# Performance work log

Hardware: AMD Instinct MI355X
Metric: run time of the kernel (lower is better)

Reference implementation:

```python
import jax, jax.numpy as jnp
import numpy as np

H, V, L = 1024, 50257, 512

def setup_inputs() -> dict:
    key = jax.random.key(0)
    ks = jax.random.split(key, 14)
    s = 0.02
    return {
        "input": jax.random.randint(ks[0], (1,), 0, V),
        "hidden": jax.random.normal(ks[1], (1, 1, H), jnp.float32),
        "encoder_outputs": jax.random.normal(ks[2], (L, H), jnp.float32),
        "emb": jax.random.normal(ks[3], (V, H), jnp.float32) * s,
        "attn_w": jax.random.normal(ks[4], (L, 2 * H), jnp.float32) * s,
        "attn_b": jnp.zeros((L,), jnp.float32),
        "comb_w": jax.random.normal(ks[5], (H, 2 * H), jnp.float32) * s,
        "comb_b": jnp.zeros((H,), jnp.float32),
        "w_ih": jax.random.normal(ks[6], (3 * H, H), jnp.float32) * s,
        "w_hh": jax.random.normal(ks[7], (3 * H, H), jnp.float32) * s,
        "b_ih": jnp.zeros((3 * H,), jnp.float32),
        "b_hh": jnp.zeros((3 * H,), jnp.float32),
        "out_w": jax.random.normal(ks[8], (V, H), jnp.float32) * s,
        "out_b": jnp.zeros((V,), jnp.float32),
    }

def reference(input, hidden, encoder_outputs, emb, attn_w, attn_b,
              comb_w, comb_b, w_ih, w_hh, b_ih, b_hh, out_w, out_b):
    # embedding lookup (dropout is identity in eval mode)
    e = emb[input]                       # (1, H)
    h0 = hidden[0]                       # (1, H)
    # attention over encoder outputs
    scores = jnp.concatenate([e, h0], axis=1) @ attn_w.T + attn_b   # (1, L)
    attn_weights = jax.nn.softmax(scores, axis=1)                    # (1, L)
    attn_applied = attn_weights @ encoder_outputs                    # (1, H)
    # combine + relu
    x = jnp.concatenate([e, attn_applied], axis=1) @ comb_w.T + comb_b
    x = jax.nn.relu(x)                   # (1, H)
    # single GRU step (PyTorch gate layout: r, z, n)
    gi = x @ w_ih.T + b_ih               # (1, 3H)
    gh = h0 @ w_hh.T + b_hh              # (1, 3H)
    i_r, i_z, i_n = jnp.split(gi, 3, axis=1)
    h_r, h_z, h_n = jnp.split(gh, 3, axis=1)
    r = jax.nn.sigmoid(i_r + h_r)
    z = jax.nn.sigmoid(i_z + h_z)
    n = jnp.tanh(i_n + r * h_n)
    h_new = (1.0 - z) * n + z * h0       # (1, H)
    # output projection + log_softmax
    logits = h_new @ out_w.T + out_b     # (1, V)
    out = jax.nn.log_softmax(logits, axis=1)
    return out, h_new[None], attn_weights
```

## Files before the change

### kernel.cpp

```cpp
#include <hip/hip_runtime.h>

#define H 1024
#define L 512
#define V 50257

__device__ __forceinline__ float wave_reduce_sum(float v) {
    #pragma unroll
    for (int o = 32; o > 0; o >>= 1) v += __shfl_xor(v, o, 64);
    return v;
}

__device__ __forceinline__ float block_reduce_sum256(float v, float* lds) {
    v = wave_reduce_sum(v);
    int wid = threadIdx.x >> 6, lane = threadIdx.x & 63;
    if (lane == 0) lds[wid] = v;
    __syncthreads();
    float r = 0.f;
    if (threadIdx.x == 0) r = lds[0] + lds[1] + lds[2] + lds[3];
    __syncthreads();
    return r;
}

__global__ void k_scores(const float* __restrict__ emb, const int* __restrict__ input,
                         const float* __restrict__ hidden, const float* __restrict__ attn_w,
                         const float* __restrict__ attn_b, float* __restrict__ scores) {
    __shared__ float lds[4];
    int l = blockIdx.x, t = threadIdx.x;
    size_t erow = (size_t)input[0] * H;
    const float4* w = (const float4*)(attn_w + (size_t)l * 2 * H);
    float4 a  = w[t];
    float4 b  = w[256 + t];
    float4 ev = ((const float4*)(emb + erow))[t];
    float4 hv = ((const float4*)hidden)[t];
    float acc = a.x*ev.x + a.y*ev.y + a.z*ev.z + a.w*ev.w
              + b.x*hv.x + b.y*hv.y + b.z*hv.z + b.w*hv.w;
    acc = block_reduce_sum256(acc, lds);
    if (t == 0) scores[l] = acc + attn_b[l];
}

__global__ void k_softmax(const float* __restrict__ scores, float* __restrict__ attn_out) {
    __shared__ float lds[8];
    int t = threadIdx.x;
    float x = scores[t];
    float m = x;
    #pragma unroll
    for (int o = 32; o > 0; o >>= 1) m = fmaxf(m, __shfl_xor(m, o, 64));
    if ((t & 63) == 0) lds[t >> 6] = m;
    __syncthreads();
    m = lds[0];
    #pragma unroll
    for (int i = 1; i < 8; ++i) m = fmaxf(m, lds[i]);
    __syncthreads();
    float e = expf(x - m);
    float s = e;
    #pragma unroll
    for (int o = 32; o > 0; o >>= 1) s += __shfl_xor(s, o, 64);
    if ((t & 63) == 0) lds[t >> 6] = s;
    __syncthreads();
    s = 0.f;
    #pragma unroll
    for (int i = 0; i < 8; ++i) s += lds[i];
    attn_out[t] = e / s;
}

__global__ void k_attn_partial(const float* __restrict__ enc, const float* __restrict__ w,
                               float* __restrict__ partial) {
    int b = blockIdx.x, t = threadIdx.x;
    float4 acc = {0.f, 0.f, 0.f, 0.f};
    for (int l = b * 16; l < b * 16 + 16; ++l) {
        float wl = w[l];
        float4 ev = ((const float4*)(enc + (size_t)l * H))[t];
        acc.x += wl * ev.x; acc.y += wl * ev.y; acc.z += wl * ev.z; acc.w += wl * ev.w;
    }
    ((float4*)(partial + (size_t)b * H))[t] = acc;
}

__global__ void k_attn_reduce(const float* __restrict__ partial, float* __restrict__ attn_applied) {
    int h = blockIdx.x * 256 + threadIdx.x;
    float s = 0.f;
    #pragma unroll 8
    for (int p = 0; p < 32; ++p) s += partial[p * H + h];
    attn_applied[h] = s;
}

__global__ void k_combine(const float* __restrict__ emb, const int* __restrict__ input,
                          const float* __restrict__ attn_applied, const float* __restrict__ comb_w,
                          const float* __restrict__ comb_b, float* __restrict__ x) {
    __shared__ float lds[4];
    int h = blockIdx.x, t = threadIdx.x;
    size_t erow = (size_t)input[0] * H;
    const float4* w = (const float4*)(comb_w + (size_t)h * 2 * H);
    float4 a  = w[t];
    float4 b  = w[256 + t];
    float4 ev = ((const float4*)(emb + erow))[t];
    float4 av = ((const float4*)attn_applied)[t];
    float acc = a.x*ev.x + a.y*ev.y + a.z*ev.z + a.w*ev.w
              + b.x*av.x + b.y*av.y + b.z*av.z + b.w*av.w;
    acc = block_reduce_sum256(acc, lds);
    if (t == 0) x[h] = fmaxf(acc + comb_b[h], 0.f);
}

__global__ void k_gigh(const float* __restrict__ w_ih, const float* __restrict__ w_hh,
                       const float* __restrict__ b_ih, const float* __restrict__ b_hh,
                       const float* __restrict__ x, const float* __restrict__ hidden,
                       float* __restrict__ gi, float* __restrict__ gh) {
    __shared__ float lds[4];
    int j = blockIdx.x, t = threadIdx.x;
    float4 wi = ((const float4*)(w_ih + (size_t)j * H))[t];
    float4 wh = ((const float4*)(w_hh + (size_t)j * H))[t];
    float4 xv = ((const float4*)x)[t];
    float4 hv = ((const float4*)hidden)[t];
    float ai = wi.x*xv.x + wi.y*xv.y + wi.z*xv.z + wi.w*xv.w;
    float ah = wh.x*hv.x + wh.y*hv.y + wh.z*hv.z + wh.w*hv.w;
    ai = block_reduce_sum256(ai, lds);
    ah = block_reduce_sum256(ah, lds);
    if (t == 0) { gi[j] = ai + b_ih[j]; gh[j] = ah + b_hh[j]; }
}

__global__ void k_gru(const float* __restrict__ gi, const float* __restrict__ gh,
                      const float* __restrict__ hidden, float* __restrict__ hnew) {
    int h = blockIdx.x * 256 + threadIdx.x;
    float r = 1.f / (1.f + expf(-(gi[h] + gh[h])));
    float z = 1.f / (1.f + expf(-(gi[H + h] + gh[H + h])));
    float n = tanhf(gi[2 * H + h] + r * gh[2 * H + h]);
    hnew[h] = (1.f - z) * n + z * hidden[h];
}

__global__ void k_logits(const float* __restrict__ out_w, const float* __restrict__ out_b,
                         const float* __restrict__ hvec, float* __restrict__ logits) {
    int lane = threadIdx.x & 63;
    int gwave = blockIdx.x * 4 + (threadIdx.x >> 6);
    int nwaves = gridDim.x * 4;
    float4 h4[4];
    #pragma unroll
    for (int j = 0; j < 4; ++j) h4[j] = ((const float4*)hvec)[j * 64 + lane];
    for (int r = gwave; r < V; r += nwaves) {
        const float4* row = (const float4*)(out_w + (size_t)r * H);
        float acc = 0.f;
        #pragma unroll
        for (int j = 0; j < 4; ++j) {
            float4 a = row[j * 64 + lane];
            acc += a.x*h4[j].x + a.y*h4[j].y + a.z*h4[j].z + a.w*h4[j].w;
        }
        acc = wave_reduce_sum(acc);
        if (lane == 0) logits[r] = acc + out_b[r];
    }
}

__global__ void k_lse_partial(const float* __restrict__ logits,
                              float* __restrict__ mpart, float* __restrict__ spart) {
    __shared__ float lm[4], ls[4];
    const int CH = (V + 63) / 64;
    int b = blockIdx.x, t = threadIdx.x;
    int start = b * CH, end = min(start + CH, V);
    float m = -INFINITY, s = 0.f;
    for (int v = start + t; v < end; v += 256) {
        float xv = logits[v];
        if (xv > m) { s = s * expf(m - xv) + 1.f; m = xv; }
        else s += expf(xv - m);
    }
    #pragma unroll
    for (int o = 32; o > 0; o >>= 1) {
        float m2 = __shfl_xor(m, o, 64), s2 = __shfl_xor(s, o, 64);
        float mm = fmaxf(m, m2);
        if (mm > -INFINITY) s = s * expf(m - mm) + s2 * expf(m2 - mm);
        m = mm;
    }
    int wid = t >> 6, lane = t & 63;
    if (lane == 0) { lm[wid] = m; ls[wid] = s; }
    __syncthreads();
    if (t == 0) {
        float M = fmaxf(fmaxf(lm[0], lm[1]), fmaxf(lm[2], lm[3]));
        float S = 0.f;
        if (M > -INFINITY) {
            #pragma unroll
            for (int i = 0; i < 4; ++i) S += ls[i] * expf(lm[i] - M);
        }
        mpart[b] = M; spart[b] = S;
    }
}

__global__ void k_finalize(const float* __restrict__ mpart, const float* __restrict__ spart,
                           float* __restrict__ out) {
    float m = -INFINITY;
    #pragma unroll 8
    for (int i = 0; i < 64; ++i) m = fmaxf(m, mpart[i]);
    float s = 0.f;
    #pragma unroll 8
    for (int i = 0; i < 64; ++i) s += spart[i] * expf(mpart[i] - m);
    float logZ = m + logf(s);
    int v = blockIdx.x * 256 + threadIdx.x;
    if (v < V) out[v] -= logZ;
}

extern "C" void kernel_launch(void* const* d_in, const int* in_sizes, int n_in,
                              void* d_out, int out_size, void* d_ws, size_t ws_size,
                              hipStream_t stream) {
    const int*   input  = (const int*)  d_in[0];
    const float* hidden = (const float*)d_in[1];
    const float* enc    = (const float*)d_in[2];
    const float* emb    = (const float*)d_in[3];
    const float* attn_w = (const float*)d_in[4];
    const float* attn_b = (const float*)d_in[5];
    const float* comb_w = (const float*)d_in[6];
    const float* comb_b = (const float*)d_in[7];
    const float* w_ih   = (const float*)d_in[8];
    const float* w_hh   = (const float*)d_in[9];
    const float* b_ih   = (const float*)d_in[10];
    const float* b_hh   = (const float*)d_in[11];
    const float* out_w  = (const float*)d_in[12];
    const float* out_b  = (const float*)d_in[13];

    float* out   = (float*)d_out;
    float* hnew  = out + V;
    float* attnw = out + V + H;

    float* ws           = (float*)d_ws;
    float* scores       = ws;
    float* partial      = ws + 512;
    float* attn_applied = ws + 33280;
    float* xbuf         = ws + 34304;
    float* gi           = ws + 35328;
    float* gh           = ws + 38400;
    float* mpart        = ws + 41472;
    float* spart        = ws + 41536;

    k_scores      <<<512, 256, 0, stream>>>(emb, input, hidden, attn_w, attn_b, scores);
    k_softmax     <<<1, 512, 0, stream>>>(scores, attnw);
    k_attn_partial<<<32, 256, 0, stream>>>(enc, attnw, partial);
    k_attn_reduce <<<4, 256, 0, stream>>>(partial, attn_applied);
    k_combine     <<<1024, 256, 0, stream>>>(emb, input, attn_applied, comb_w, comb_b, xbuf);
    k_gigh        <<<3072, 256, 0, stream>>>(w_ih, w_hh, b_ih, b_hh, xbuf, hidden, gi, gh);
    k_gru         <<<4, 256, 0, stream>>>(gi, gh, hidden, hnew);
    k_logits      <<<2048, 256, 0, stream>>>(out_w, out_b, hnew, out);
    k_lse_partial <<<64, 256, 0, stream>>>(out, mpart, spart);
    k_finalize    <<<(V + 255) / 256, 256, 0, stream>>>(mpart, spart, out);
}
```

Baseline: 71.25 us.

## Fuse attention softmax/apply, GRU gates, and logits with LSE partials

Cuts the pipeline from ten launches to six. Softmax and the attention-weighted sum go into one kernel where every block recomputes the softmax. The GRU gate matvecs and the cell update go into one kernel per hidden unit, and the per-block max/sum-exp is computed inside the logits kernel, so the separate LSE pass over the logits is gone. This removes launch gaps and extra global round trips. In exchange, the finalize kernel now reduces 2048 partials in every block, and each attention block redundantly redoes the softmax.

```diff
diff --git a/kernel.cpp b/kernel.cpp
--- a/kernel.cpp
+++ b/kernel.cpp
@@ -3,22 +3,12 @@
 #define H 1024
 #define L 512
 #define V 50257
+#define LOGIT_BLOCKS 2048
 
 __device__ __forceinline__ float wave_reduce_sum(float v) {
     #pragma unroll
     for (int o = 32; o > 0; o >>= 1) v += __shfl_xor(v, o, 64);
     return v;
-}
-
-__device__ __forceinline__ float block_reduce_sum256(float v, float* lds) {
-    v = wave_reduce_sum(v);
-    int wid = threadIdx.x >> 6, lane = threadIdx.x & 63;
-    if (lane == 0) lds[wid] = v;
-    __syncthreads();
-    float r = 0.f;
-    if (threadIdx.x == 0) r = lds[0] + lds[1] + lds[2] + lds[3];
-    __syncthreads();
-    return r;
 }
 
 __global__ void k_scores(const float* __restrict__ emb, const int* __restrict__ input,
@@ -34,53 +24,54 @@
     float4 hv = ((const float4*)hidden)[t];
     float acc = a.x*ev.x + a.y*ev.y + a.z*ev.z + a.w*ev.w
               + b.x*hv.x + b.y*hv.y + b.z*hv.z + b.w*hv.w;
-    acc = block_reduce_sum256(acc, lds);
-    if (t == 0) scores[l] = acc + attn_b[l];
-}
-
-__global__ void k_softmax(const float* __restrict__ scores, float* __restrict__ attn_out) {
-    __shared__ float lds[8];
-    int t = threadIdx.x;
-    float x = scores[t];
-    float m = x;
+    acc = wave_reduce_sum(acc);
+    int wid = t >> 6, lane = t & 63;
+    if (lane == 0) lds[wid] = acc;
+    __syncthreads();
+    if (t == 0) scores[l] = lds[0] + lds[1] + lds[2] + lds[3] + attn_b[l];
+}
+
+__global__ void k_attn(const float* __restrict__ scores, const float* __restrict__ enc,
+                       float* __restrict__ attn_out, float* __restrict__ attn_applied) {
+    __shared__ float w[512];
+    __shared__ float red[4];
+    __shared__ float acc_lds[256];
+    __shared__ float sM, sS;
+    int t = threadIdx.x, lane = t & 63, wid = t >> 6;
+    float s0 = scores[t], s1 = scores[t + 256];
+    float m = fmaxf(s0, s1);
     #pragma unroll
     for (int o = 32; o > 0; o >>= 1) m = fmaxf(m, __shfl_xor(m, o, 64));
-    if ((t & 63) == 0) lds[t >> 6] = m;
-    __syncthreads();
-    m = lds[0];
-    #pragma unroll
-    for (int i = 1; i < 8; ++i) m = fmaxf(m, lds[i]);
-    __syncthreads();
-    float e = expf(x - m);
-    float s = e;
-    #pragma unroll
-    for (int o = 32; o > 0; o >>= 1) s += __shfl_xor(s, o, 64);
-    if ((t & 63) == 0) lds[t >> 6] = s;
-    __syncthreads();
-    s = 0.f;
-    #pragma unroll
-    for (int i = 0; i < 8; ++i) s += lds[i];
-    attn_out[t] = e / s;
-}
-
-__global__ void k_attn_partial(const float* __restrict__ enc, const float* __restrict__ w,
-                               float* __restrict__ partial) {
-    int b = blockIdx.x, t = threadIdx.x;
-    float4 acc = {0.f, 0.f, 0.f, 0.f};
-    for (int l = b * 16; l < b * 16 + 16; ++l) {
-        float wl = w[l];
-        float4 ev = ((const float4*)(enc + (size_t)l * H))[t];
-        acc.x += wl * ev.x; acc.y += wl * ev.y; acc.z += wl * ev.z; acc.w += wl * ev.w;
-    }
-    ((float4*)(partial + (size_t)b * H))[t] = acc;
-}
-
-__global__ void k_attn_reduce(const float* __restrict__ partial, float* __restrict__ attn_applied) {
-    int h = blockIdx.x * 256 + threadIdx.x;
-    float s = 0.f;
+    if (lane == 0) red[wid] = m;
+    __syncthreads();
+    if (t == 0) sM = fmaxf(fmaxf(red[0], red[1]), fmaxf(red[2], red[3]));
+    __syncthreads();
+    float M = sM;
+    float e0 = expf(s0 - M), e1 = expf(s1 - M);
+    float s = e0 + e1;
+    s = wave_reduce_sum(s);
+    if (lane == 0) red[wid] = s;
+    __syncthreads();
+    if (t == 0) sS = red[0] + red[1] + red[2] + red[3];
+    __syncthreads();
+    float inv = 1.f / sS;
+    w[t] = e0 * inv; w[t + 256] = e1 * inv;
+    __syncthreads();
+    if (blockIdx.x == 0) { attn_out[t] = w[t]; attn_out[t + 256] = w[t + 256]; }
+    int col = blockIdx.x * 16 + (t & 15);
+    int rc  = t >> 4;
+    float acc = 0.f;
     #pragma unroll 8
-    for (int p = 0; p < 32; ++p) s += partial[p * H + h];
-    attn_applied[h] = s;
+    for (int l = rc; l < 512; l += 16)
+        acc += w[l] * enc[(size_t)l * H + col];
+    acc_lds[t] = acc;
+    __syncthreads();
+    #pragma unroll
+    for (int st = 128; st >= 16; st >>= 1) {
+        if (t < st) acc_lds[t] += acc_lds[t + st];
+        __syncthreads();
+    }
+    if (t < 16) attn_applied[blockIdx.x * 16 + t] = acc_lds[t];
 }
 
 __global__ void k_combine(const float* __restrict__ emb, const int* __restrict__ input,
@@ -96,44 +87,62 @@
     float4 av = ((const float4*)attn_applied)[t];
     float acc = a.x*ev.x + a.y*ev.y + a.z*ev.z + a.w*ev.w
               + b.x*av.x + b.y*av.y + b.z*av.z + b.w*av.w;
-    acc = block_reduce_sum256(acc, lds);
-    if (t == 0) x[h] = fmaxf(acc + comb_b[h], 0.f);
-}
-
-__global__ void k_gigh(const float* __restrict__ w_ih, const float* __restrict__ w_hh,
-                       const float* __restrict__ b_ih, const float* __restrict__ b_hh,
-                       const float* __restrict__ x, const float* __restrict__ hidden,
-                       float* __restrict__ gi, float* __restrict__ gh) {
-    __shared__ float lds[4];
-    int j = blockIdx.x, t = threadIdx.x;
-    float4 wi = ((const float4*)(w_ih + (size_t)j * H))[t];
-    float4 wh = ((const float4*)(w_hh + (size_t)j * H))[t];
+    acc = wave_reduce_sum(acc);
+    int wid = t >> 6, lane = t & 63;
+    if (lane == 0) lds[wid] = acc;
+    __syncthreads();
+    if (t == 0) x[h] = fmaxf(lds[0] + lds[1] + lds[2] + lds[3] + comb_b[h], 0.f);
+}
+
+__global__ void k_gru_fused(const float* __restrict__ w_ih, const float* __restrict__ w_hh,
+                            const float* __restrict__ b_ih, const float* __restrict__ b_hh,
+                            const float* __restrict__ x, const float* __restrict__ hidden,
+                            float* __restrict__ hnew) {
+    __shared__ float lds[4][6];
+    int h = blockIdx.x, t = threadIdx.x, lane = t & 63, wid = t >> 6;
     float4 xv = ((const float4*)x)[t];
     float4 hv = ((const float4*)hidden)[t];
-    float ai = wi.x*xv.x + wi.y*xv.y + wi.z*xv.z + wi.w*xv.w;
-    float ah = wh.x*hv.x + wh.y*hv.y + wh.z*hv.z + wh.w*hv.w;
-    ai = block_reduce_sum256(ai, lds);
-    ah = block_reduce_sum256(ah, lds);
-    if (t == 0) { gi[j] = ai + b_ih[j]; gh[j] = ah + b_hh[j]; }
-}
-
-__global__ void k_gru(const float* __restrict__ gi, const float* __restrict__ gh,
-                      const float* __restrict__ hidden, float* __restrict__ hnew) {
-    int h = blockIdx.x * 256 + threadIdx.x;
-    float r = 1.f / (1.f + expf(-(gi[h] + gh[h])));
-    float z = 1.f / (1.f + expf(-(gi[H + h] + gh[H + h])));
-    float n = tanhf(gi[2 * H + h] + r * gh[2 * H + h]);
-    hnew[h] = (1.f - z) * n + z * hidden[h];
-}
-
-__global__ void k_logits(const float* __restrict__ out_w, const float* __restrict__ out_b,
-                         const float* __restrict__ hvec, float* __restrict__ logits) {
-    int lane = threadIdx.x & 63;
-    int gwave = blockIdx.x * 4 + (threadIdx.x >> 6);
-    int nwaves = gridDim.x * 4;
+    const float* rows[6] = {
+        w_ih + (size_t)h * H, w_ih + (size_t)(H + h) * H, w_ih + (size_t)(2 * H + h) * H,
+        w_hh + (size_t)h * H, w_hh + (size_t)(H + h) * H, w_hh + (size_t)(2 * H + h) * H };
+    float acc[6];
+    #pragma unroll
+    for (int k = 0; k < 6; ++k) {
+        float4 wv = ((const float4*)rows[k])[t];
+        float4 v  = (k < 3) ? xv : hv;
+        acc[k] = wv.x*v.x + wv.y*v.y + wv.z*v.z + wv.w*v.w;
+        acc[k] = wave_reduce_sum(acc[k]);
+    }
+    if (lane == 0) {
+        #pragma unroll
+        for (int k = 0; k < 6; ++k) lds[wid][k] = acc[k];
+    }
+    __syncthreads();
+    if (t == 0) {
+        float g[6];
+        #pragma unroll
+        for (int k = 0; k < 6; ++k) g[k] = lds[0][k] + lds[1][k] + lds[2][k] + lds[3][k];
+        float ir = g[0] + b_ih[h],         hr = g[3] + b_hh[h];
+        float iz = g[1] + b_ih[H + h],     hz = g[4] + b_hh[H + h];
+        float in_ = g[2] + b_ih[2 * H + h], hn = g[5] + b_hh[2 * H + h];
+        float r = 1.f / (1.f + expf(-(ir + hr)));
+        float z = 1.f / (1.f + expf(-(iz + hz)));
+        float n = tanhf(in_ + r * hn);
+        hnew[h] = (1.f - z) * n + z * hidden[h];
+    }
+}
+
+__global__ void k_logits_lse(const float* __restrict__ out_w, const float* __restrict__ out_b,
+                             const float* __restrict__ hvec, float* __restrict__ logits,
+                             float* __restrict__ mpart, float* __restrict__ spart) {
+    __shared__ float lm[4], ls[4];
+    int lane = threadIdx.x & 63, wid = threadIdx.x >> 6;
+    int gwave = blockIdx.x * 4 + wid;
+    const int nwaves = LOGIT_BLOCKS * 4;
     float4 h4[4];
     #pragma unroll
     for (int j = 0; j < 4; ++j) h4[j] = ((const float4*)hvec)[j * 64 + lane];
+    float m = -INFINITY, s = 0.f;
     for (int r = gwave; r < V; r += nwaves) {
         const float4* row = (const float4*)(out_w + (size_t)r * H);
         float acc = 0.f;
@@ -143,54 +152,55 @@
             acc += a.x*h4[j].x + a.y*h4[j].y + a.z*h4[j].z + a.w*h4[j].w;
         }
         acc = wave_reduce_sum(acc);
-        if (lane == 0) logits[r] = acc + out_b[r];
-    }
-}
-
-__global__ void k_lse_partial(const float* __restrict__ logits,
-                              float* __restrict__ mpart, float* __restrict__ spart) {
-    __shared__ float lm[4], ls[4];
-    const int CH = (V + 63) / 64;
-    int b = blockIdx.x, t = threadIdx.x;
-    int start = b * CH, end = min(start + CH, V);
-    float m = -INFINITY, s = 0.f;
-    for (int v = start + t; v < end; v += 256) {
-        float xv = logits[v];
-        if (xv > m) { s = s * expf(m - xv) + 1.f; m = xv; }
-        else s += expf(xv - m);
-    }
-    #pragma unroll
-    for (int o = 32; o > 0; o >>= 1) {
-        float m2 = __shfl_xor(m, o, 64), s2 = __shfl_xor(s, o, 64);
-        float mm = fmaxf(m, m2);
-        if (mm > -INFINITY) s = s * expf(m - mm) + s2 * expf(m2 - mm);
-        m = mm;
-    }
-    int wid = t >> 6, lane = t & 63;
+        float logit = acc + out_b[r];
+        if (lane == 0) logits[r] = logit;
+        if (logit > m) { s = s * expf(m - logit) + 1.f; m = logit; }
+        else           { s += expf(logit - m); }
+    }
     if (lane == 0) { lm[wid] = m; ls[wid] = s; }
     __syncthreads();
-    if (t == 0) {
+    if (threadIdx.x == 0) {
         float M = fmaxf(fmaxf(lm[0], lm[1]), fmaxf(lm[2], lm[3]));
         float S = 0.f;
         if (M > -INFINITY) {
             #pragma unroll
             for (int i = 0; i < 4; ++i) S += ls[i] * expf(lm[i] - M);
         }
-        mpart[b] = M; spart[b] = S;
+        mpart[blockIdx.x] = M; spart[blockIdx.x] = S;
     }
 }
 
 __global__ void k_finalize(const float* __restrict__ mpart, const float* __restrict__ spart,
                            float* __restrict__ out) {
-    float m = -INFINITY;
-    #pragma unroll 8
-    for (int i = 0; i < 64; ++i) m = fmaxf(m, mpart[i]);
-    float s = 0.f;
-    #pragma unroll 8
-    for (int i = 0; i < 64; ++i) s += spart[i] * expf(mpart[i] - m);
-    float logZ = m + logf(s);
-    int v = blockIdx.x * 256 + threadIdx.x;
-    if (v < V) out[v] -= logZ;
+    __shared__ float lm[4], ls[4];
+    __shared__ float sLogZ;
+    int t = threadIdx.x, lane = t & 63, wid = t >> 6;
+    float m = -INFINITY, s = 0.f;
+    for (int i = t; i < LOGIT_BLOCKS; i += 256) {
+        float m2 = mpart[i], s2 = spart[i];
+        float mm = fmaxf(m, m2);
+        if (mm > -INFINITY) s = s * expf(m - mm) + s2 * expf(m2 - mm);
+        m = mm;
+    }
+    #pragma unroll
+    for (int o = 32; o > 0; o >>= 1) {
+        float m2 = __shfl_xor(m, o, 64), s2 = __shfl_xor(s, o, 64);
+        float mm = fmaxf(m, m2);
+        if (mm > -INFINITY) s = s * expf(m - mm) + s2 * expf(m2 - mm);
+        m = mm;
+    }
+    if (lane == 0) { lm[wid] = m; ls[wid] = s; }
+    __syncthreads();
+    if (t == 0) {
+        float M = fmaxf(fmaxf(lm[0], lm[1]), fmaxf(lm[2], lm[3]));
+        float S = 0.f;
+        #pragma unroll
+        for (int i = 0; i < 4; ++i) S += ls[i] * expf(lm[i] - M);
+        sLogZ = M + logf(S);
+    }
+    __syncthreads();
+    int v = blockIdx.x * 256 + t;
+    if (v < V) out[v] -= sLogZ;
 }
 
 extern "C" void kernel_launch(void* const* d_in, const int* in_sizes, int n_in,
@@ -217,22 +227,15 @@
 
     float* ws           = (float*)d_ws;
     float* scores       = ws;
-    float* partial      = ws + 512;
-    float* attn_applied = ws + 33280;
-    float* xbuf         = ws + 34304;
-    float* gi           = ws + 35328;
-    float* gh           = ws + 38400;
-    float* mpart        = ws + 41472;
-    float* spart        = ws + 41536;
-
-    k_scores      <<<512, 256, 0, stream>>>(emb, input, hidden, attn_w, attn_b, scores);
-    k_softmax     <<<1, 512, 0, stream>>>(scores, attnw);
-    k_attn_partial<<<32, 256, 0, stream>>>(enc, attnw, partial);
-    k_attn_reduce <<<4, 256, 0, stream>>>(partial, attn_applied);
-    k_combine     <<<1024, 256, 0, stream>>>(emb, input, attn_applied, comb_w, comb_b, xbuf);
-    k_gigh        <<<3072, 256, 0, stream>>>(w_ih, w_hh, b_ih, b_hh, xbuf, hidden, gi, gh);
-    k_gru         <<<4, 256, 0, stream>>>(gi, gh, hidden, hnew);
-    k_logits      <<<2048, 256, 0, stream>>>(out_w, out_b, hnew, out);
-    k_lse_partial <<<64, 256, 0, stream>>>(out, mpart, spart);
-    k_finalize    <<<(V + 255) / 256, 256, 0, stream>>>(mpart, spart, out);
-}
+    float* attn_applied = ws + 512;
+    float* xbuf         = ws + 1536;
+    float* mpart        = ws + 2560;
+    float* spart        = ws + 4608;
+
+    k_scores     <<<512, 256, 0, stream>>>(emb, input, hidden, attn_w, attn_b, scores);
+    k_attn       <<<64, 256, 0, stream>>>(scores, enc, attnw, attn_applied);
+    k_combine    <<<1024, 256, 0, stream>>>(emb, input, attn_applied, comb_w, comb_b, xbuf);
+    k_gru_fused  <<<1024, 256, 0, stream>>>(w_ih, w_hh, b_ih, b_hh, xbuf, hidden, hnew);
+    k_logits_lse <<<LOGIT_BLOCKS, 256, 0, stream>>>(out_w, out_b, hnew, out, mpart, spart);
+    k_finalize   <<<(V + 255) / 256, 256, 0, stream>>>(mpart, spart, out);
+}
```

Measured after the change: 61.44 us. 1.16x faster.
